# Kernel tuning notes

Measured on AMD Instinct MI355X. Metric: run time of the kernel, lower is better.

## Reference

```python
import jax, jax.numpy as jnp
import numpy as np

N = 50000
E = 1600000
IN_C = 128
HID = 64
OUT_C = 64
EPS = 1e-5
NEG_SLOPE = 0.01  # nn.LeakyReLU default


def setup_inputs() -> dict:
    key = jax.random.key(0)
    ks = jax.random.split(key, 8)
    x = jax.random.normal(ks[0], (N, IN_C), dtype=jnp.float32)
    x_e = jnp.zeros((1,), dtype=jnp.float32)  # unused by the module
    edge_index = jax.random.randint(ks[1], (2, E), 0, N, dtype=jnp.int64)
    # Parameters (torch default-ish init scale)
    s1 = 1.0 / np.sqrt(IN_C)
    W1 = jax.random.uniform(ks[2], (HID, IN_C), jnp.float32, -s1, s1)
    b1 = jax.random.uniform(ks[3], (HID,), jnp.float32, -s1, s1)
    gamma = jnp.ones((HID,), jnp.float32)
    beta = jnp.zeros((HID,), jnp.float32)
    s2 = 1.0 / np.sqrt(HID)
    W2 = jax.random.uniform(ks[4], (OUT_C, HID), jnp.float32, -s2, s2)
    b2 = jax.random.uniform(ks[5], (OUT_C,), jnp.float32, -s2, s2)
    return {"x": x, "x_e": x_e, "edge_index": edge_index,
            "W1": W1, "b1": b1, "gamma": gamma, "beta": beta,
            "W2": W2, "b2": b2}


def reference(x, x_e, edge_index, W1, b1, gamma, beta, W2, b2):
    # dropout: identity in eval mode
    h = jax.nn.leaky_relu(x @ W1.T + b1, negative_slope=NEG_SLOPE)  # [N, HID]
    # LayerNorm over last dim
    mu = jnp.mean(h, axis=-1, keepdims=True)
    var = jnp.mean(jnp.square(h - mu), axis=-1, keepdims=True)
    h = (h - mu) * jax.lax.rsqrt(var + EPS) * gamma + beta
    # gather over src edges, scatter-min into dst nodes
    src, dst = edge_index[0], edge_index[1]
    agg = jax.ops.segment_min(h[src], dst, num_segments=N)  # [N, HID]
    # nodes with no incoming edge: segment_min -> +inf; PyG fills 0
    agg = jnp.where(jnp.isinf(agg), 0.0, agg)
    out = agg @ W2.T + b2  # [N, OUT_C]
    return out
```

## Files before the change

kernel.cpp:

```cpp
#include <hip/hip_runtime.h>
#include <hip/hip_fp16.h>
#include <cstdint>
#include <math.h>

#define IN_C 128
#define HID 64
#define OUT_C 64
#define EPS_LN 1e-5f
#define NEG_SLOPE 0.01f

#define NBUCKET 1024
#define ROWS 49
#define CAP 2048
#define EPB 4096

typedef __attribute__((ext_vector_type(8))) short short8;
typedef __attribute__((ext_vector_type(4))) float f32x4;
typedef __attribute__((ext_vector_type(2))) _Float16 f16x2;
typedef __attribute__((ext_vector_type(8))) _Float16 f16x8;

__device__ __forceinline__ unsigned pack_hi(float f0, float f1) {
    return (__float_as_uint(f0) >> 16) | (__float_as_uint(f1) & 0xFFFF0000u);
}
__device__ __forceinline__ float hi_part(float f) {
    return __uint_as_float(__float_as_uint(f) & 0xFFFF0000u);
}
__device__ __forceinline__ unsigned hmin2u(unsigned a, unsigned b) {
    union { unsigned u; f16x2 v; } ua, ub, r;
    ua.u = a; ub.u = b;
    r.v = __builtin_elementwise_min(ua.v, ub.v);
    return r.u;
}

__global__ __launch_bounds__(256) void mlp_ln_mfma_kernel(
    const float* __restrict__ x, const float* __restrict__ W1,
    const float* __restrict__ b1, const float* __restrict__ gamma,
    const float* __restrict__ beta, unsigned short* __restrict__ h16,
    unsigned* __restrict__ cursor, int N)
{
    __shared__ unsigned whi[64 * 68];
    __shared__ unsigned wlo[64 * 68];
    __shared__ unsigned short hT[64 * 66];

    const int tid = threadIdx.x;

    if (blockIdx.x == 0) {
        for (int i = tid; i < NBUCKET; i += 256) cursor[i * 16] = 0;
    }

    {
        int r = tid >> 2, q = tid & 3;
        const float4* wr4 = (const float4*)(W1 + r * IN_C + q * 32);
#pragma unroll
        for (int p = 0; p < 8; ++p) {
            float4 f = wr4[p];
            unsigned h0 = pack_hi(f.x, f.y);
            unsigned h1 = pack_hi(f.z, f.w);
            unsigned l0 = pack_hi(f.x - hi_part(f.x), f.y - hi_part(f.y));
            unsigned l1 = pack_hi(f.z - hi_part(f.z), f.w - hi_part(f.w));
            whi[r * 68 + q * 16 + 2 * p]     = h0;
            whi[r * 68 + q * 16 + 2 * p + 1] = h1;
            wlo[r * 68 + q * 16 + 2 * p]     = l0;
            wlo[r * 68 + q * 16 + 2 * p + 1] = l1;
        }
    }
    __syncthreads();

    const int lane = tid & 63;
    const int w    = tid >> 6;
    const int col  = lane & 15;
    const int g    = lane >> 4;
    const int nodeBase0 = blockIdx.x * 64;
    const int nodeBase  = nodeBase0 + w * 16;

    f32x4 acc[4];
#pragma unroll
    for (int t = 0; t < 4; ++t) acc[t] = (f32x4){0.f, 0.f, 0.f, 0.f};

    const int nodeCl = min(nodeBase + col, N - 1);

#pragma unroll
    for (int ks = 0; ks < 4; ++ks) {
        const float* xp = x + (size_t)nodeCl * IN_C + ks * 32 + g * 8;
        float4 fa = *(const float4*)xp;
        float4 fb = *(const float4*)(xp + 4);
        float f[8] = {fa.x, fa.y, fa.z, fa.w, fb.x, fb.y, fb.z, fb.w};
        union { unsigned u[4]; short8 s; } Ah, Al;
#pragma unroll
        for (int p = 0; p < 4; ++p) {
            float f0 = f[2 * p], f1 = f[2 * p + 1];
            Ah.u[p] = pack_hi(f0, f1);
            Al.u[p] = pack_hi(f0 - hi_part(f0), f1 - hi_part(f1));
        }
#pragma unroll
        for (int t = 0; t < 4; ++t) {
            const short8* bh = (const short8*)&whi[(t * 16 + col) * 68 + ks * 16 + g * 4];
            const short8* bl = (const short8*)&wlo[(t * 16 + col) * 68 + ks * 16 + g * 4];
            short8 Bh = *bh;
            short8 Bl = *bl;
            acc[t] = __builtin_amdgcn_mfma_f32_16x16x32_bf16(Ah.s, Bh, acc[t], 0, 0, 0);
            acc[t] = __builtin_amdgcn_mfma_f32_16x16x32_bf16(Ah.s, Bl, acc[t], 0, 0, 0);
            acc[t] = __builtin_amdgcn_mfma_f32_16x16x32_bf16(Al.s, Bh, acc[t], 0, 0, 0);
        }
    }

    float b1v[4], gv[4], bv[4];
#pragma unroll
    for (int t = 0; t < 4; ++t) {
        b1v[t] = b1[t * 16 + col];
        gv[t]  = gamma[t * 16 + col];
        bv[t]  = beta[t * 16 + col];
    }
    float val[4][4];
#pragma unroll
    for (int t = 0; t < 4; ++t)
#pragma unroll
        for (int r = 0; r < 4; ++r) {
            float v = acc[t][r] + b1v[t];
            val[t][r] = v > 0.f ? v : v * NEG_SLOPE;
        }

    float s[4], q[4];
#pragma unroll
    for (int r = 0; r < 4; ++r) {
        s[r] = val[0][r] + val[1][r] + val[2][r] + val[3][r];
        q[r] = fmaf(val[0][r], val[0][r],
               fmaf(val[1][r], val[1][r],
               fmaf(val[2][r], val[2][r], val[3][r] * val[3][r])));
    }
#pragma unroll
    for (int off = 1; off < 16; off <<= 1) {
#pragma unroll
        for (int r = 0; r < 4; ++r) {
            s[r] += __shfl_xor(s[r], off, 64);
            q[r] += __shfl_xor(q[r], off, 64);
        }
    }
    float mu[4], rstd[4];
#pragma unroll
    for (int r = 0; r < 4; ++r) {
        mu[r] = s[r] * (1.f / 64.f);
        float var = q[r] * (1.f / 64.f) - mu[r] * mu[r];
        rstd[r] = rsqrtf(var + EPS_LN);
    }
#pragma unroll
    for (int t = 0; t < 4; ++t)
#pragma unroll
        for (int r = 0; r < 4; ++r) {
            float hn = (val[t][r] - mu[r]) * rstd[r] * gv[t] + bv[t];
            int nodeL = w * 16 + g * 4 + r;
            hT[nodeL * 66 + t * 16 + col] = __half_as_ushort(__float2half(hn));
        }
    __syncthreads();

    {
        int nodeL = tid >> 2, part = tid & 3;
        int node = nodeBase0 + nodeL;
        if (node < N) {
            const unsigned* hrow = (const unsigned*)hT;
            unsigned tmp[8];
#pragma unroll
            for (int i = 0; i < 8; ++i) tmp[i] = hrow[nodeL * 33 + part * 8 + i];
            unsigned* gp = (unsigned*)h16 + (size_t)node * 32 + part * 8;
            *(uint4*)gp       = (uint4){tmp[0], tmp[1], tmp[2], tmp[3]};
            *(uint4*)(gp + 4) = (uint4){tmp[4], tmp[5], tmp[6], tmp[7]};
        }
    }
}

__global__ __launch_bounds__(512) void bucket_scatter_kernel(
    const int* __restrict__ ei, unsigned* __restrict__ cursor ,
    unsigned* __restrict__ pairs, int E)
{
    __shared__ unsigned hist[NBUCKET];
    __shared__ unsigned run_start[NBUCKET];
    __shared__ unsigned c2[NBUCKET];
    __shared__ unsigned gbase[NBUCKET];
    __shared__ unsigned pre[512];
    __shared__ unsigned staged[EPB];
    __shared__ unsigned short bof[EPB];

    const int tid = threadIdx.x;
    const int base = blockIdx.x * EPB;

    hist[tid] = 0;
    hist[tid + 512] = 0;
    __syncthreads();

    unsigned pk[8];
    unsigned short bk[8];
#pragma unroll
    for (int k = 0; k < 8; ++k) {
        int e = base + k * 512 + tid;
        if (e < E) {
            unsigned src = (unsigned)ei[e];
            unsigned dst = (unsigned)ei[E + e];
            unsigned b = dst & (NBUCKET - 1);
            pk[k] = src | ((dst >> 10) << 16);
            bk[k] = (unsigned short)b;
            atomicAdd(&hist[b], 1u);
        } else {
            bk[k] = 0xFFFFu;
        }
    }
    __syncthreads();

    unsigned sA = hist[2 * tid], sB = hist[2 * tid + 1];
    pre[tid] = sA + sB;
    __syncthreads();
    for (int off = 1; off < 512; off <<= 1) {
        unsigned v = (tid >= off) ? pre[tid - off] : 0u;
        __syncthreads();
        pre[tid] += v;
        __syncthreads();
    }
    unsigned excl = pre[tid] - (sA + sB);
    run_start[2 * tid] = excl;
    run_start[2 * tid + 1] = excl + sA;
    c2[2 * tid] = excl;
    c2[2 * tid + 1] = excl + sA;
    if (sA) gbase[2 * tid] = atomicAdd(&cursor[(2 * tid) * 16], sA);
    if (sB) gbase[2 * tid + 1] = atomicAdd(&cursor[(2 * tid + 1) * 16], sB);
    __syncthreads();

#pragma unroll
    for (int k = 0; k < 8; ++k) {
        if (bk[k] != 0xFFFFu) {
            unsigned pos = atomicAdd(&c2[bk[k]], 1u);
            staged[pos] = pk[k];
            bof[pos] = bk[k];
        }
    }
    __syncthreads();

    int total = min(EPB, E - base);
    for (int i = tid; i < total; i += 512) {
        unsigned b = bof[i];
        unsigned local = gbase[b] + ((unsigned)i - run_start[b]);
        if (local < CAP) pairs[(size_t)b * CAP + local] = staged[i];
    }
}

__global__ __launch_bounds__(512) void bucket_reduce_gemm_kernel(
    const unsigned* __restrict__ hp ,
    const unsigned* __restrict__ cursor, const unsigned* __restrict__ pairs,
    const float* __restrict__ W2, const float* __restrict__ b2,
    float* __restrict__ out, int N)
{
    __shared__ unsigned rec_sorted[CAP];
    __shared__ unsigned accP[64 * 36];
    __shared__ unsigned w2h[64 * 36];
    __shared__ unsigned rhist[64], rstart[64], rc[64];

    const int tid  = threadIdx.x;
    const int lane = tid & 63;
    const int wid  = tid >> 6;
    const unsigned b = blockIdx.x;
    const unsigned INITV = 0x7C007C00u;

    if (tid < 64) rhist[tid] = 0;
    for (int i = tid; i < 64 * 36; i += 512) accP[i] = INITV;
    for (int i = tid; i < 64 * 32; i += 512) {
        int n = i >> 5, p = i & 5 * 6 + 1;
        p = i & 31;
        float f0 = W2[n * 64 + 2 * p], f1 = W2[n * 64 + 2 * p + 1];
        unsigned u0 = (unsigned)__half_as_ushort(__float2half(f0));
        unsigned u1 = (unsigned)__half_as_ushort(__float2half(f1));
        w2h[n * 36 + p] = u0 | (u1 << 16);
    }

    const unsigned cnt = min(cursor[b * 16], (unsigned)CAP);
    unsigned myrec[4];
#pragma unroll
    for (int k = 0; k < 4; ++k) {
        unsigned i = (unsigned)tid + k * 512;
        myrec[k] = (i < cnt) ? pairs[(size_t)b * CAP + i] : 0xFFFFFFFFu;
    }
    __syncthreads();

#pragma unroll
    for (int k = 0; k < 4; ++k)
        if (myrec[k] != 0xFFFFFFFFu) atomicAdd(&rhist[myrec[k] >> 16], 1u);
    __syncthreads();

    if (wid == 0) {
        unsigned v = (lane < ROWS) ? rhist[lane] : 0u;
        unsigned inc = v;
#pragma unroll
        for (int off = 1; off < 64; off <<= 1) {
            unsigned u = __shfl_up(inc, (unsigned)off, 64);
            if (lane >= off) inc += u;
        }
        if (lane < ROWS) { rstart[lane] = inc - v; rc[lane] = inc - v; }
    }
    __syncthreads();

#pragma unroll
    for (int k = 0; k < 4; ++k)
        if (myrec[k] != 0xFFFFFFFFu) {
            unsigned pos = atomicAdd(&rc[myrec[k] >> 16], 1u);
            rec_sorted[pos] = myrec[k];
        }
    __syncthreads();

    const unsigned sub = (unsigned)(lane >> 3);
    const unsigned cg  = (unsigned)(lane & 7);
    for (int r = wid; r < ROWS; r += 8) {
        unsigned L = rhist[r];
        if (L == 0) continue;
        unsigned st = rstart[r];
        uint4 acc = {INITV, INITV, INITV, INITV};
        for (unsigned bb = 0; bb < L; bb += 8) {
            unsigned k = bb + sub;
            unsigned rec = rec_sorted[st + min(k, L - 1)];
            unsigned node = rec & 0xFFFFu;
            uint4 v = *(const uint4*)(hp + (size_t)node * 32 + cg * 4);
            acc.x = hmin2u(acc.x, v.x);
            acc.y = hmin2u(acc.y, v.y);
            acc.z = hmin2u(acc.z, v.z);
            acc.w = hmin2u(acc.w, v.w);
        }
#pragma unroll
        for (int off = 8; off < 64; off <<= 1) {
            acc.x = hmin2u(acc.x, (unsigned)__shfl_xor((int)acc.x, off, 64));
            acc.y = hmin2u(acc.y, (unsigned)__shfl_xor((int)acc.y, off, 64));
            acc.z = hmin2u(acc.z, (unsigned)__shfl_xor((int)acc.z, off, 64));
            acc.w = hmin2u(acc.w, (unsigned)__shfl_xor((int)acc.w, off, 64));
        }
        if (lane < 8)
            *(uint4*)&accP[r * 36 + cg * 4] = acc;
    }
    __syncthreads();

    for (int i = tid; i < 64 * 32; i += 512) {
        int r = i >> 5, p = i & 31;
        unsigned v = accP[r * 36 + p];
        unsigned lo = v & 0xFFFFu, hi = v >> 16;
        if (lo == 0x7C00u) lo = 0;
        if (hi == 0x7C00u) hi = 0;
        accP[r * 36 + p] = lo | (hi << 16);
    }
    __syncthreads();

    {
        const int col = lane & 15;
        const int g   = lane >> 4;
        const int mtile = wid >> 1;
        f16x8 afrag[2];
#pragma unroll
        for (int kt = 0; kt < 2; ++kt)
            afrag[kt] = *(const f16x8*)&accP[(mtile * 16 + col) * 36 + kt * 16 + g * 4];
#pragma unroll
        for (int nn = 0; nn < 2; ++nn) {
            int ntile = (wid & 1) * 2 + nn;
            f16x8 b0 = *(const f16x8*)&w2h[(ntile * 16 + col) * 36 + 0 * 16 + g * 4];
            f16x8 b1f = *(const f16x8*)&w2h[(ntile * 16 + col) * 36 + 1 * 16 + g * 4];
            f32x4 c = {0.f, 0.f, 0.f, 0.f};
            c = __builtin_amdgcn_mfma_f32_16x16x32_f16(afrag[0], b0, c, 0, 0, 0);
            c = __builtin_amdgcn_mfma_f32_16x16x32_f16(afrag[1], b1f, c, 0, 0, 0);
            float b2v = b2[ntile * 16 + col];
#pragma unroll
            for (int r4 = 0; r4 < 4; ++r4) {
                int m = mtile * 16 + g * 4 + r4;
                int dst = (m << 10) | (int)b;
                if (m < ROWS && dst < N)
                    out[(size_t)dst * OUT_C + ntile * 16 + col] = c[r4] + b2v;
            }
        }
    }
}

extern "C" void kernel_launch(void* const* d_in, const int* in_sizes, int n_in,
                              void* d_out, int out_size, void* d_ws, size_t ws_size,
                              hipStream_t stream) {
    const float* x     = (const float*)d_in[0];
    const int*   ei    = (const int*)d_in[2];
    const float* W1    = (const float*)d_in[3];
    const float* b1    = (const float*)d_in[4];
    const float* gamma = (const float*)d_in[5];
    const float* beta  = (const float*)d_in[6];
    const float* W2    = (const float*)d_in[7];
    const float* b2    = (const float*)d_in[8];
    float* out = (float*)d_out;

    const int N = in_sizes[0] / IN_C;
    const int E = in_sizes[2] / 2;

    unsigned short* h16 = (unsigned short*)d_ws;
    unsigned* pairs  = (unsigned*)(h16 + (size_t)N * HID);
    unsigned* cursor = pairs + (size_t)NBUCKET * CAP;

    const int mlp_blocks = (N + 63) / 64;
    mlp_ln_mfma_kernel<<<mlp_blocks, 256, 0, stream>>>(
        x, W1, b1, gamma, beta, h16, cursor, N);

    const int scat_blocks = (E + EPB - 1) / EPB;
    bucket_scatter_kernel<<<scat_blocks, 512, 0, stream>>>(ei, cursor, pairs, E);

    bucket_reduce_gemm_kernel<<<NBUCKET, 512, 0, stream>>>(
        (const unsigned*)h16, cursor, pairs, W2, b2, out, N);
}
```

Baseline: 147.2 us.

## Merge MLP and bucket scatter into one interleaved launch, unroll gather loop

The MLP+LayerNorm and edge bucket-scatter kernels are combined into a single launch whose blocks alternate between the two roles. This lets the independent stages run concurrently and removes one kernel boundary. The MLP blocks now hold 512 threads and 128 nodes, and shared memory is one union buffer. Other changes: the scatter prefix scan uses wave shuffles instead of a barrier-heavy LDS scan, cursor zeroing moves to a hipMemsetAsync, and the reduce kernel's gather loop keeps two accumulators to allow more loads in flight. The extra memset launch and heavier LDS use per block may offset part of the gain.

```diff
diff --git a/kernel.cpp b/kernel.cpp
--- a/kernel.cpp
+++ b/kernel.cpp
@@ -32,212 +32,217 @@
     return r.u;
 }
 
-__global__ __launch_bounds__(256) void mlp_ln_mfma_kernel(
+__global__ __launch_bounds__(512) void mlp_and_scatter_kernel(
     const float* __restrict__ x, const float* __restrict__ W1,
     const float* __restrict__ b1, const float* __restrict__ gamma,
     const float* __restrict__ beta, unsigned short* __restrict__ h16,
-    unsigned* __restrict__ cursor, int N)
+    const int* __restrict__ ei, unsigned* __restrict__ cursor ,
+    unsigned* __restrict__ pairs, int N, int E, int NB_MLP, int NB_SCAT)
 {
-    __shared__ unsigned whi[64 * 68];
-    __shared__ unsigned wlo[64 * 68];
-    __shared__ unsigned short hT[64 * 66];
+    __shared__ __align__(16) unsigned smem[12928];
 
     const int tid = threadIdx.x;
-
-    if (blockIdx.x == 0) {
-        for (int i = tid; i < NBUCKET; i += 256) cursor[i * 16] = 0;
-    }
-
-    {
-        int r = tid >> 2, q = tid & 3;
-        const float4* wr4 = (const float4*)(W1 + r * IN_C + q * 32);
-#pragma unroll
-        for (int p = 0; p < 8; ++p) {
-            float4 f = wr4[p];
-            unsigned h0 = pack_hi(f.x, f.y);
-            unsigned h1 = pack_hi(f.z, f.w);
-            unsigned l0 = pack_hi(f.x - hi_part(f.x), f.y - hi_part(f.y));
-            unsigned l1 = pack_hi(f.z - hi_part(f.z), f.w - hi_part(f.w));
-            whi[r * 68 + q * 16 + 2 * p]     = h0;
-            whi[r * 68 + q * 16 + 2 * p + 1] = h1;
-            wlo[r * 68 + q * 16 + 2 * p]     = l0;
-            wlo[r * 68 + q * 16 + 2 * p + 1] = l1;
-        }
-    }
-    __syncthreads();
-
-    const int lane = tid & 63;
-    const int w    = tid >> 6;
-    const int col  = lane & 15;
-    const int g    = lane >> 4;
-    const int nodeBase0 = blockIdx.x * 64;
-    const int nodeBase  = nodeBase0 + w * 16;
-
-    f32x4 acc[4];
-#pragma unroll
-    for (int t = 0; t < 4; ++t) acc[t] = (f32x4){0.f, 0.f, 0.f, 0.f};
-
-    const int nodeCl = min(nodeBase + col, N - 1);
-
-#pragma unroll
-    for (int ks = 0; ks < 4; ++ks) {
-        const float* xp = x + (size_t)nodeCl * IN_C + ks * 32 + g * 8;
-        float4 fa = *(const float4*)xp;
-        float4 fb = *(const float4*)(xp + 4);
-        float f[8] = {fa.x, fa.y, fa.z, fa.w, fb.x, fb.y, fb.z, fb.w};
-        union { unsigned u[4]; short8 s; } Ah, Al;
-#pragma unroll
-        for (int p = 0; p < 4; ++p) {
-            float f0 = f[2 * p], f1 = f[2 * p + 1];
-            Ah.u[p] = pack_hi(f0, f1);
-            Al.u[p] = pack_hi(f0 - hi_part(f0), f1 - hi_part(f1));
-        }
+    const int bx  = blockIdx.x;
+
+    const int nmin2 = 2 * min(NB_MLP, NB_SCAT);
+    bool do_mlp; int id;
+    if (bx < nmin2) { do_mlp = (bx & 1) == 0; id = bx >> 1; }
+    else {
+        int rr = bx - nmin2;
+        do_mlp = (NB_MLP > NB_SCAT);
+        id = (nmin2 >> 1) + rr;
+    }
+
+    if (do_mlp) {
+        unsigned* whi = smem;
+        unsigned* wlo = smem + 4352;
+        unsigned short* hT = (unsigned short*)(smem + 8704);
+
+        if (tid < 256) {
+            int r = tid >> 2, q = tid & 3;
+            const float4* wr4 = (const float4*)(W1 + r * IN_C + q * 32);
+#pragma unroll
+            for (int p = 0; p < 8; ++p) {
+                float4 f = wr4[p];
+                whi[r * 68 + q * 16 + 2 * p]     = pack_hi(f.x, f.y);
+                whi[r * 68 + q * 16 + 2 * p + 1] = pack_hi(f.z, f.w);
+                wlo[r * 68 + q * 16 + 2 * p]     = pack_hi(f.x - hi_part(f.x), f.y - hi_part(f.y));
+                wlo[r * 68 + q * 16 + 2 * p + 1] = pack_hi(f.z - hi_part(f.z), f.w - hi_part(f.w));
+            }
+        }
+        __syncthreads();
+
+        const int lane = tid & 63;
+        const int w    = tid >> 6;
+        const int col  = lane & 15;
+        const int g    = lane >> 4;
+        const int nodeBase0 = id * 128;
+        const int nodeBase  = nodeBase0 + w * 16;
+
+        f32x4 acc[4];
+#pragma unroll
+        for (int t = 0; t < 4; ++t) acc[t] = (f32x4){0.f, 0.f, 0.f, 0.f};
+
+        const int nodeCl = min(nodeBase + col, N - 1);
+
+#pragma unroll
+        for (int ks = 0; ks < 4; ++ks) {
+            const float* xp = x + (size_t)nodeCl * IN_C + ks * 32 + g * 8;
+            float4 fa = *(const float4*)xp;
+            float4 fb = *(const float4*)(xp + 4);
+            float f[8] = {fa.x, fa.y, fa.z, fa.w, fb.x, fb.y, fb.z, fb.w};
+            union { unsigned u[4]; short8 s; } Ah, Al;
+#pragma unroll
+            for (int p = 0; p < 4; ++p) {
+                float f0 = f[2 * p], f1 = f[2 * p + 1];
+                Ah.u[p] = pack_hi(f0, f1);
+                Al.u[p] = pack_hi(f0 - hi_part(f0), f1 - hi_part(f1));
+            }
+#pragma unroll
+            for (int t = 0; t < 4; ++t) {
+                short8 Bh = *(const short8*)&whi[(t * 16 + col) * 68 + ks * 16 + g * 4];
+                short8 Bl = *(const short8*)&wlo[(t * 16 + col) * 68 + ks * 16 + g * 4];
+                acc[t] = __builtin_amdgcn_mfma_f32_16x16x32_bf16(Ah.s, Bh, acc[t], 0, 0, 0);
+                acc[t] = __builtin_amdgcn_mfma_f32_16x16x32_bf16(Ah.s, Bl, acc[t], 0, 0, 0);
+                acc[t] = __builtin_amdgcn_mfma_f32_16x16x32_bf16(Al.s, Bh, acc[t], 0, 0, 0);
+            }
+        }
+
+        float b1v[4], gv[4], bv[4];
 #pragma unroll
         for (int t = 0; t < 4; ++t) {
-            const short8* bh = (const short8*)&whi[(t * 16 + col) * 68 + ks * 16 + g * 4];
-            const short8* bl = (const short8*)&wlo[(t * 16 + col) * 68 + ks * 16 + g * 4];
-            short8 Bh = *bh;
-            short8 Bl = *bl;
-            acc[t] = __builtin_amdgcn_mfma_f32_16x16x32_bf16(Ah.s, Bh, acc[t], 0, 0, 0);
-            acc[t] = __builtin_amdgcn_mfma_f32_16x16x32_bf16(Ah.s, Bl, acc[t], 0, 0, 0);
-            acc[t] = __builtin_amdgcn_mfma_f32_16x16x32_bf16(Al.s, Bh, acc[t], 0, 0, 0);
-        }
-    }
-
-    float b1v[4], gv[4], bv[4];
-#pragma unroll
-    for (int t = 0; t < 4; ++t) {
-        b1v[t] = b1[t * 16 + col];
-        gv[t]  = gamma[t * 16 + col];
-        bv[t]  = beta[t * 16 + col];
-    }
-    float val[4][4];
-#pragma unroll
-    for (int t = 0; t < 4; ++t)
+            b1v[t] = b1[t * 16 + col];
+            gv[t]  = gamma[t * 16 + col];
+            bv[t]  = beta[t * 16 + col];
+        }
+        float val[4][4];
+#pragma unroll
+        for (int t = 0; t < 4; ++t)
+#pragma unroll
+            for (int r = 0; r < 4; ++r) {
+                float v = acc[t][r] + b1v[t];
+                val[t][r] = v > 0.f ? v : v * NEG_SLOPE;
+            }
+
+        float s[4], q[4];
 #pragma unroll
         for (int r = 0; r < 4; ++r) {
-            float v = acc[t][r] + b1v[t];
-            val[t][r] = v > 0.f ? v : v * NEG_SLOPE;
-        }
-
-    float s[4], q[4];
-#pragma unroll
-    for (int r = 0; r < 4; ++r) {
-        s[r] = val[0][r] + val[1][r] + val[2][r] + val[3][r];
-        q[r] = fmaf(val[0][r], val[0][r],
-               fmaf(val[1][r], val[1][r],
-               fmaf(val[2][r], val[2][r], val[3][r] * val[3][r])));
-    }
-#pragma unroll
-    for (int off = 1; off < 16; off <<= 1) {
+            s[r] = val[0][r] + val[1][r] + val[2][r] + val[3][r];
+            q[r] = fmaf(val[0][r], val[0][r],
+                   fmaf(val[1][r], val[1][r],
+                   fmaf(val[2][r], val[2][r], val[3][r] * val[3][r])));
+        }
+#pragma unroll
+        for (int off = 1; off < 16; off <<= 1) {
+#pragma unroll
+            for (int r = 0; r < 4; ++r) {
+                s[r] += __shfl_xor(s[r], off, 64);
+                q[r] += __shfl_xor(q[r], off, 64);
+            }
+        }
+        float mu[4], rstd[4];
 #pragma unroll
         for (int r = 0; r < 4; ++r) {
-            s[r] += __shfl_xor(s[r], off, 64);
-            q[r] += __shfl_xor(q[r], off, 64);
-        }
-    }
-    float mu[4], rstd[4];
-#pragma unroll
-    for (int r = 0; r < 4; ++r) {
-        mu[r] = s[r] * (1.f / 64.f);
-        float var = q[r] * (1.f / 64.f) - mu[r] * mu[r];
-        rstd[r] = rsqrtf(var + EPS_LN);
-    }
-#pragma unroll
-    for (int t = 0; t < 4; ++t)
-#pragma unroll
-        for (int r = 0; r < 4; ++r) {
-            float hn = (val[t][r] - mu[r]) * rstd[r] * gv[t] + bv[t];
-            int nodeL = w * 16 + g * 4 + r;
-            hT[nodeL * 66 + t * 16 + col] = __half_as_ushort(__float2half(hn));
-        }
-    __syncthreads();
-
-    {
-        int nodeL = tid >> 2, part = tid & 3;
-        int node = nodeBase0 + nodeL;
-        if (node < N) {
-            const unsigned* hrow = (const unsigned*)hT;
-            unsigned tmp[8];
-#pragma unroll
-            for (int i = 0; i < 8; ++i) tmp[i] = hrow[nodeL * 33 + part * 8 + i];
-            unsigned* gp = (unsigned*)h16 + (size_t)node * 32 + part * 8;
-            *(uint4*)gp       = (uint4){tmp[0], tmp[1], tmp[2], tmp[3]};
-            *(uint4*)(gp + 4) = (uint4){tmp[4], tmp[5], tmp[6], tmp[7]};
-        }
-    }
-}
-
-__global__ __launch_bounds__(512) void bucket_scatter_kernel(
-    const int* __restrict__ ei, unsigned* __restrict__ cursor ,
-    unsigned* __restrict__ pairs, int E)
-{
-    __shared__ unsigned hist[NBUCKET];
-    __shared__ unsigned run_start[NBUCKET];
-    __shared__ unsigned c2[NBUCKET];
-    __shared__ unsigned gbase[NBUCKET];
-    __shared__ unsigned pre[512];
-    __shared__ unsigned staged[EPB];
-    __shared__ unsigned short bof[EPB];
-
-    const int tid = threadIdx.x;
-    const int base = blockIdx.x * EPB;
-
-    hist[tid] = 0;
-    hist[tid + 512] = 0;
-    __syncthreads();
-
-    unsigned pk[8];
-    unsigned short bk[8];
-#pragma unroll
-    for (int k = 0; k < 8; ++k) {
-        int e = base + k * 512 + tid;
-        if (e < E) {
-            unsigned src = (unsigned)ei[e];
-            unsigned dst = (unsigned)ei[E + e];
-            unsigned b = dst & (NBUCKET - 1);
-            pk[k] = src | ((dst >> 10) << 16);
-            bk[k] = (unsigned short)b;
-            atomicAdd(&hist[b], 1u);
-        } else {
-            bk[k] = 0xFFFFu;
-        }
-    }
-    __syncthreads();
-
-    unsigned sA = hist[2 * tid], sB = hist[2 * tid + 1];
-    pre[tid] = sA + sB;
-    __syncthreads();
-    for (int off = 1; off < 512; off <<= 1) {
-        unsigned v = (tid >= off) ? pre[tid - off] : 0u;
-        __syncthreads();
-        pre[tid] += v;
-        __syncthreads();
-    }
-    unsigned excl = pre[tid] - (sA + sB);
-    run_start[2 * tid] = excl;
-    run_start[2 * tid + 1] = excl + sA;
-    c2[2 * tid] = excl;
-    c2[2 * tid + 1] = excl + sA;
-    if (sA) gbase[2 * tid] = atomicAdd(&cursor[(2 * tid) * 16], sA);
-    if (sB) gbase[2 * tid + 1] = atomicAdd(&cursor[(2 * tid + 1) * 16], sB);
-    __syncthreads();
-
-#pragma unroll
-    for (int k = 0; k < 8; ++k) {
-        if (bk[k] != 0xFFFFu) {
-            unsigned pos = atomicAdd(&c2[bk[k]], 1u);
-            staged[pos] = pk[k];
-            bof[pos] = bk[k];
-        }
-    }
-    __syncthreads();
-
-    int total = min(EPB, E - base);
-    for (int i = tid; i < total; i += 512) {
-        unsigned b = bof[i];
-        unsigned local = gbase[b] + ((unsigned)i - run_start[b]);
-        if (local < CAP) pairs[(size_t)b * CAP + local] = staged[i];
+            mu[r] = s[r] * (1.f / 64.f);
+            float var = q[r] * (1.f / 64.f) - mu[r] * mu[r];
+            rstd[r] = rsqrtf(var + EPS_LN);
+        }
+#pragma unroll
+        for (int t = 0; t < 4; ++t)
+#pragma unroll
+            for (int r = 0; r < 4; ++r) {
+                float hn = (val[t][r] - mu[r]) * rstd[r] * gv[t] + bv[t];
+                int nodeL = w * 16 + g * 4 + r;
+                hT[nodeL * 66 + t * 16 + col] = __half_as_ushort(__float2half(hn));
+            }
+        __syncthreads();
+
+        {
+            int nodeL = tid >> 2, part = tid & 3;
+            int node = nodeBase0 + nodeL;
+            if (node < N) {
+                const unsigned* hrow = (const unsigned*)hT;
+                unsigned tmp[8];
+#pragma unroll
+                for (int i = 0; i < 8; ++i) tmp[i] = hrow[nodeL * 33 + part * 8 + i];
+                unsigned* gp = (unsigned*)h16 + (size_t)node * 32 + part * 8;
+                *(uint4*)gp       = (uint4){tmp[0], tmp[1], tmp[2], tmp[3]};
+                *(uint4*)(gp + 4) = (uint4){tmp[4], tmp[5], tmp[6], tmp[7]};
+            }
+        }
+    } else {
+        unsigned* staged    = smem;
+        unsigned short* bof = (unsigned short*)(smem + 4096);
+        unsigned* hist      = smem + 6144;
+        unsigned* run_start = smem + 7168;
+        unsigned* c2        = smem + 8192;
+        unsigned* gbase     = smem + 9216;
+        unsigned* wsum      = smem + 10240;
+
+        const int base = id * EPB;
+        const int lane = tid & 63;
+        const int wv   = tid >> 6;
+
+        hist[tid] = 0;
+        hist[tid + 512] = 0;
+        __syncthreads();
+
+        unsigned pk[8];
+        unsigned short bk[8];
+#pragma unroll
+        for (int k = 0; k < 8; ++k) {
+            int e = base + k * 512 + tid;
+            if (e < E) {
+                unsigned src = (unsigned)ei[e];
+                unsigned dst = (unsigned)ei[E + e];
+                unsigned b = dst & (NBUCKET - 1);
+                pk[k] = src | ((dst >> 10) << 16);
+                bk[k] = (unsigned short)b;
+                atomicAdd(&hist[b], 1u);
+            } else {
+                bk[k] = 0xFFFFu;
+            }
+        }
+        __syncthreads();
+
+        unsigned sA = hist[2 * tid], sB = hist[2 * tid + 1];
+        unsigned sv = sA + sB;
+        unsigned inc = sv;
+#pragma unroll
+        for (int off = 1; off < 64; off <<= 1) {
+            unsigned u = __shfl_up(inc, (unsigned)off, 64);
+            if (lane >= off) inc += u;
+        }
+        if (lane == 63) wsum[wv] = inc;
+        __syncthreads();
+        unsigned wbase = 0;
+        for (int i = 0; i < wv; ++i) wbase += wsum[i];
+        unsigned excl = wbase + inc - sv;
+
+        run_start[2 * tid] = excl;
+        run_start[2 * tid + 1] = excl + sA;
+        c2[2 * tid] = excl;
+        c2[2 * tid + 1] = excl + sA;
+        if (sA) gbase[2 * tid] = atomicAdd(&cursor[(2 * tid) * 16], sA);
+        if (sB) gbase[2 * tid + 1] = atomicAdd(&cursor[(2 * tid + 1) * 16], sB);
+        __syncthreads();
+
+#pragma unroll
+        for (int k = 0; k < 8; ++k) {
+            if (bk[k] != 0xFFFFu) {
+                unsigned pos = atomicAdd(&c2[bk[k]], 1u);
+                staged[pos] = pk[k];
+                bof[pos] = bk[k];
+            }
+        }
+        __syncthreads();
+
+        int total = min(EPB, E - base);
+        for (int i = tid; i < total; i += 512) {
+            unsigned b = bof[i];
+            unsigned local = gbase[b] + ((unsigned)i - run_start[b]);
+            if (local < CAP) pairs[(size_t)b * CAP + local] = staged[i];
+        }
     }
 }
 
@@ -261,8 +266,7 @@
     if (tid < 64) rhist[tid] = 0;
     for (int i = tid; i < 64 * 36; i += 512) accP[i] = INITV;
     for (int i = tid; i < 64 * 32; i += 512) {
-        int n = i >> 5, p = i & 5 * 6 + 1;
-        p = i & 31;
+        int n = i >> 5, p = i & 31;
         float f0 = W2[n * 64 + 2 * p], f1 = W2[n * 64 + 2 * p + 1];
         unsigned u0 = (unsigned)__half_as_ushort(__float2half(f0));
         unsigned u1 = (unsigned)__half_as_ushort(__float2half(f1));
@@ -309,17 +313,22 @@
         unsigned L = rhist[r];
         if (L == 0) continue;
         unsigned st = rstart[r];
-        uint4 acc = {INITV, INITV, INITV, INITV};
-        for (unsigned bb = 0; bb < L; bb += 8) {
-            unsigned k = bb + sub;
-            unsigned rec = rec_sorted[st + min(k, L - 1)];
-            unsigned node = rec & 0xFFFFu;
-            uint4 v = *(const uint4*)(hp + (size_t)node * 32 + cg * 4);
-            acc.x = hmin2u(acc.x, v.x);
-            acc.y = hmin2u(acc.y, v.y);
-            acc.z = hmin2u(acc.z, v.z);
-            acc.w = hmin2u(acc.w, v.w);
-        }
+        uint4 acc  = {INITV, INITV, INITV, INITV};
+        uint4 acc2 = {INITV, INITV, INITV, INITV};
+        for (unsigned bb = 0; bb < L; bb += 16) {
+            unsigned k1 = min(bb + sub, L - 1);
+            unsigned k2 = min(bb + 8 + sub, L - 1);
+            unsigned n1 = rec_sorted[st + k1] & 0xFFFFu;
+            unsigned n2 = rec_sorted[st + k2] & 0xFFFFu;
+            uint4 v1 = *(const uint4*)(hp + (size_t)n1 * 32 + cg * 4);
+            uint4 v2 = *(const uint4*)(hp + (size_t)n2 * 32 + cg * 4);
+            acc.x  = hmin2u(acc.x,  v1.x); acc.y  = hmin2u(acc.y,  v1.y);
+            acc.z  = hmin2u(acc.z,  v1.z); acc.w  = hmin2u(acc.w,  v1.w);
+            acc2.x = hmin2u(acc2.x, v2.x); acc2.y = hmin2u(acc2.y, v2.y);
+            acc2.z = hmin2u(acc2.z, v2.z); acc2.w = hmin2u(acc2.w, v2.w);
+        }
+        acc.x = hmin2u(acc.x, acc2.x); acc.y = hmin2u(acc.y, acc2.y);
+        acc.z = hmin2u(acc.z, acc2.z); acc.w = hmin2u(acc.w, acc2.w);
 #pragma unroll
         for (int off = 8; off < 64; off <<= 1) {
             acc.x = hmin2u(acc.x, (unsigned)__shfl_xor((int)acc.x, off, 64));
@@ -353,7 +362,7 @@
 #pragma unroll
         for (int nn = 0; nn < 2; ++nn) {
             int ntile = (wid & 1) * 2 + nn;
-            f16x8 b0 = *(const f16x8*)&w2h[(ntile * 16 + col) * 36 + 0 * 16 + g * 4];
+            f16x8 b0  = *(const f16x8*)&w2h[(ntile * 16 + col) * 36 + 0 * 16 + g * 4];
             f16x8 b1f = *(const f16x8*)&w2h[(ntile * 16 + col) * 36 + 1 * 16 + g * 4];
             f32x4 c = {0.f, 0.f, 0.f, 0.f};
             c = __builtin_amdgcn_mfma_f32_16x16x32_f16(afrag[0], b0, c, 0, 0, 0);
@@ -390,12 +399,12 @@
     unsigned* pairs  = (unsigned*)(h16 + (size_t)N * HID);
     unsigned* cursor = pairs + (size_t)NBUCKET * CAP;
 
-    const int mlp_blocks = (N + 63) / 64;
-    mlp_ln_mfma_kernel<<<mlp_blocks, 256, 0, stream>>>(
-        x, W1, b1, gamma, beta, h16, cursor, N);
-
-    const int scat_blocks = (E + EPB - 1) / EPB;
-    bucket_scatter_kernel<<<scat_blocks, 512, 0, stream>>>(ei, cursor, pairs, E);
+    hipMemsetAsync(cursor, 0, (size_t)NBUCKET * 16 * sizeof(unsigned), stream);
+
+    const int NB_MLP  = (N + 127) / 128;
+    const int NB_SCAT = (E + EPB - 1) / EPB;
+    mlp_and_scatter_kernel<<<NB_MLP + NB_SCAT, 512, 0, stream>>>(
+        x, W1, b1, gamma, beta, h16, ei, cursor, pairs, N, E, NB_MLP, NB_SCAT);
 
     bucket_reduce_gemm_kernel<<<NBUCKET, 512, 0, stream>>>(
         (const unsigned*)h16, cursor, pairs, W2, b2, out, N);
```

After: 141.7 us. 1.04x faster.
